# Kernel optimization log

Hardware: AMD Instinct MI355X
Metric: run time of the kernel (lower is better)

Reference implementation:

```python
import jax, jax.numpy as jnp
from jax import lax
import numpy as np

B, T, C, V, E, H, OC = 1024, 32, 14, 21128, 200, 50, 8


def gru(x, Wih, Whh, bih, bhh):
    # x: [N, T, E] -> hiddens [N, T, H]; torch nn.GRU gate order (r, z, n)
    Hd = Whh.shape[1]
    xp = jnp.einsum('nte,ge->ntg', x, Wih) + bih  # [N, T, 3H]
    h0 = jnp.zeros((x.shape[0], Hd), x.dtype)

    def step(h, xt):
        gh = h @ Whh.T + bhh
        r = jax.nn.sigmoid(xt[:, :Hd] + gh[:, :Hd])
        z = jax.nn.sigmoid(xt[:, Hd:2 * Hd] + gh[:, Hd:2 * Hd])
        n = jnp.tanh(xt[:, 2 * Hd:] + r * gh[:, 2 * Hd:])
        h_new = (1.0 - z) * n + z * h
        return h_new, h_new

    _, hs = lax.scan(step, h0, jnp.swapaxes(xp, 0, 1))
    return jnp.swapaxes(hs, 0, 1)


def setup_inputs():
    key = jax.random.key(0)
    ks = jax.random.split(key, 32)
    s = 0.1
    inp = {
        'contexts_indices': jax.random.randint(ks[0], (B, T), 0, V),
        'candidates_indices': jax.random.randint(ks[1], (B, C, T), 0, V),
        'y_dev': jax.random.uniform(ks[2], (B, C), dtype=jnp.float32),
        'emb': jax.random.normal(ks[3], (V, E), dtype=jnp.float32),
        'A': jax.random.normal(ks[4], (H, H), dtype=jnp.float32) * s,
        'Wih_c': jax.random.normal(ks[5], (3 * H, E), dtype=jnp.float32) * s,
        'Whh_c': jax.random.normal(ks[6], (3 * H, H), dtype=jnp.float32) * s,
        'bih_c': jnp.zeros((3 * H,), jnp.float32),
        'bhh_c': jnp.zeros((3 * H,), jnp.float32),
        'Wih_r': jax.random.normal(ks[7], (3 * H, E), dtype=jnp.float32) * s,
        'Whh_r': jax.random.normal(ks[8], (3 * H, H), dtype=jnp.float32) * s,
        'bih_r': jnp.zeros((3 * H,), jnp.float32),
        'bhh_r': jnp.zeros((3 * H,), jnp.float32),
        'conv_w': jax.random.normal(ks[9], (OC, 2, 3, 3), dtype=jnp.float32) * s,
        'Wih2': jax.random.normal(ks[10], (3 * H, OC * 10 * 10), dtype=jnp.float32) * s,
        'Whh2': jax.random.normal(ks[11], (3 * H, H), dtype=jnp.float32) * s,
        'bih2': jnp.zeros((3 * H,), jnp.float32),
        'bhh2': jnp.zeros((3 * H,), jnp.float32),
        'fc1_w': jax.random.normal(ks[12], (100, C * H), dtype=jnp.float32) * s,
        'fc1_b': jnp.zeros((100,), jnp.float32),
        'fc2_w': jax.random.normal(ks[13], (C, 100), dtype=jnp.float32) * s,
        'fc2_b': jnp.zeros((C,), jnp.float32),
    }
    return inp


def reference(contexts_indices, candidates_indices, y_dev, emb, A,
              Wih_c, Whh_c, bih_c, bhh_c, Wih_r, Whh_r, bih_r, bhh_r,
              conv_w, Wih2, Whh2, bih2, bhh2, fc1_w, fc1_b, fc2_w, fc2_b):
    b = contexts_indices.shape[0]
    ctx = contexts_indices[:, None, :]                      # [B,1,T]
    ctx_emb = emb[ctx]                                      # [B,1,T,E] (dropout = identity in eval)
    cand_emb = emb[candidates_indices]                      # [B,C,T,E]

    ctx_h = gru(ctx_emb.reshape(-1, T, E), Wih_c, Whh_c, bih_c, bhh_c).reshape(b, 1, T, H)
    cand_h = gru(cand_emb.reshape(-1, T, E), Wih_r, Whh_r, bih_r, bhh_r).reshape(b, C, T, H)

    M1 = jnp.einsum('btph,bcqh->btcpq', ctx_emb, cand_emb)  # [B,1,C,T,T]
    ctx_hA = jnp.einsum('btij,jk->btik', ctx_h, A)
    M2 = jnp.einsum('btph,bcqh->btcpq', ctx_hA, cand_h)

    # faithful to torch: stack on dim 2 then row-major view(-1, 2, T, T)
    M = jnp.stack([M1, M2], axis=2).reshape(-1, 2, T, T)    # [B*C, 2, T, T]

    conv = lax.conv_general_dilated(M, conv_w, (1, 1), 'VALID',
                                    dimension_numbers=('NCHW', 'OIHW', 'NCHW'))  # [B*C, OC, 30, 30]
    pooled = lax.reduce_window(conv, -jnp.inf, lax.max,
                               (1, 1, 3, 3), (1, 1, 3, 3), 'VALID')              # [B*C, OC, 10, 10]

    feats = pooled.reshape(b, C, OC * 10 * 10)              # [B, C, 800]
    Hs = gru(feats, Wih2, Whh2, bih2, bhh2)                 # [B, C, H]
    flat = Hs.reshape(b, -1)                                # [B, C*H]

    hid = jax.nn.relu(flat @ fc1_w.T + fc1_b)
    log_probs = jax.nn.log_softmax(hid @ fc2_w.T + fc2_b, axis=-1)  # softmax then log
    kl = jnp.where(y_dev > 0, y_dev * (jnp.log(y_dev) - log_probs), 0.0)
    return jnp.mean(kl)
```

## Files before the change

kernel.cpp:

```cpp
#include <hip/hip_runtime.h>
#include <math.h>

typedef unsigned short u16;
typedef short s16;
typedef u16 u16x8 __attribute__((ext_vector_type(8)));
typedef s16 short8v __attribute__((ext_vector_type(8)));
typedef float f32x4 __attribute__((ext_vector_type(4)));

__device__ __forceinline__ float b2f(u16 u) {
    return __uint_as_float(((unsigned)u) << 16);
}
__device__ __forceinline__ u16 f2b(float f) {
    unsigned u = __float_as_uint(f);
    unsigned r = (u + 0x7FFFu + ((u >> 16) & 1u)) >> 16;
    return (u16)r;
}

__global__ __launch_bounds__(256) void k_cvt_all(
    const float* __restrict__ emb, u16* __restrict__ embh,
    const float* __restrict__ wcf, u16* __restrict__ wch,
    const float* __restrict__ wrf, u16* __restrict__ wrh,
    const float* __restrict__ w2f, u16* __restrict__ w2h)
{
    long j = (long)blockIdx.x * 256 + threadIdx.x;
    if (j < 1056400) {
        float4 v = ((const float4*)emb)[j];
        *(ushort4*)(embh + j * 4) = make_ushort4(f2b(v.x), f2b(v.y), f2b(v.z), f2b(v.w));
        return;
    }
    j -= 1056400;
    if (j < 7500) {
        float4 v = ((const float4*)wcf)[j];
        *(ushort4*)(wch + j * 4) = make_ushort4(f2b(v.x), f2b(v.y), f2b(v.z), f2b(v.w));
        return;
    }
    j -= 7500;
    if (j < 7500) {
        float4 v = ((const float4*)wrf)[j];
        *(ushort4*)(wrh + j * 4) = make_ushort4(f2b(v.x), f2b(v.y), f2b(v.z), f2b(v.w));
        return;
    }
    j -= 7500;
    if (j < 120000) {
        int jj = (int)(j / 800), k = (int)(j % 800);
        int p = k >> 3, oc = k & 7;
        w2h[jj * 800 + k] = f2b(w2f[jj * 800 + oc * 100 + p]);
    }
}

__global__ __launch_bounds__(256) void k_projmm2(
    const u16* __restrict__ embh, const u16* __restrict__ wc,
    const u16* __restrict__ wr, const float* __restrict__ bc,
    const float* __restrict__ br, u16* __restrict__ outc,
    u16* __restrict__ outr, int V)
{
    __shared__ s16 Ab[2048];
    __shared__ s16 Bb[2560];
    __shared__ float bhL[160];
    const int t = threadIdx.x;
    const int w = t >> 6, l = t & 63, lg = l >> 4, lr = l & 15;
    int id = blockIdx.x;
    const int half = (id >= 662) ? 1 : 0;
    id -= half * 662;
    const u16* wh = half ? wr : wc;
    const float* bias = half ? br : bc;
    u16* outp = half ? outr : outc;
    const int mb = id >> 1, nb = id & 1;
    const long rowbase = (long)mb * 64;
    const int colbase = nb * 80;
    if (t < 160) bhL[t] = (t < 150) ? bias[t] : 0.f;

    f32x4 acc[5];
#pragma unroll
    for (int i = 0; i < 5; ++i) acc[i] = (f32x4){0,0,0,0};

    for (int ch = 0; ch < 7; ++ch) {
        __syncthreads();
        {
            int kc = t >> 6, row = t & 63;
            long grow = rowbase + row; if (grow >= V) grow = V - 1;
            int k0 = ch * 32 + kc * 8;
            short8v v = {0,0,0,0,0,0,0,0};
            if (k0 < 200) v = *(const short8v*)(embh + grow * 200 + k0);
            *(short8v*)&Ab[t * 8] = v;
        }
        for (int it = t; it < 320; it += 256) {
            int kc = it / 80, col = it % 80;
            int gcol = colbase + col;
            int k0 = ch * 32 + kc * 8;
            short8v v = {0,0,0,0,0,0,0,0};
            if (gcol < 150 && k0 < 200)
                v = *(const short8v*)(wh + (size_t)gcol * 200 + k0);
            *(short8v*)&Bb[it * 8] = v;
        }
        __syncthreads();
        short8v a = *(short8v*)&Ab[(lg * 64 + w * 16 + lr) * 8];
#pragma unroll
        for (int ct = 0; ct < 5; ++ct) {
            short8v bv = *(short8v*)&Bb[(lg * 80 + ct * 16 + lr) * 8];
            acc[ct] = __builtin_amdgcn_mfma_f32_16x16x32_bf16(a, bv, acc[ct], 0, 0, 0);
        }
    }
#pragma unroll
    for (int ct = 0; ct < 5; ++ct) {
        int gcol = colbase + ct * 16 + lr;
        if (gcol < 150) {
#pragma unroll
            for (int rr = 0; rr < 4; ++rr) {
                long row = rowbase + w * 16 + lg * 4 + rr;
                outp[row * 152 + gcol] = f2b(acc[ct][rr] + bhL[gcol]);
            }
        }
    }
}

template<int MODE, int SEQS>
__device__ __forceinline__ void gru_body(
    char* sm, const void* __restrict__ xp_, const int* __restrict__ idx,
    const float* __restrict__ Whh, const float* __restrict__ bhh,
    void* __restrict__ hs_, int T, long blk)
{
    s16*   hbuf = (s16*)sm;
    float* ghL  = (float*)(sm + 2048);
    float* hL   = (float*)(sm + 2048 + SEQS * 640);
    float* bhL  = (float*)(sm + 2048 + SEQS * 848);
    u16*   xraw = (u16*)(sm + 2048 + SEQS * 848 + 608);
    const int t = threadIdx.x;
    const int w = t >> 6, l = t & 63, lg = l >> 4, lr = l & 15;
    constexpr int HST = (MODE == 2) ? 56 : 50;
    constexpr int XROW = SEQS * 152;
    u16*   xbH = xraw;
    float* xbF = (float*)xraw;

    for (int li = t; li < 1024; li += 256) hbuf[li] = 0;
    for (int e = t; e < SEQS * 52; e += 256) hL[e] = 0.f;
    if (t < 152) bhL[t] = (t < 150) ? bhh[t] : 0.f;

    const int te_0 = (w * 3     > 9) ? 9 : w * 3;
    const int te_1 = (w * 3 + 1 > 9) ? 9 : w * 3 + 1;
    const int te_2 = (w * 3 + 2 > 9) ? 9 : w * 3 + 2;
    short8v B00 = {0,0,0,0,0,0,0,0}, B01 = B00, B10 = B00, B11 = B00, B20 = B00, B21 = B00;
    {
        int cols[3] = { te_0 * 16 + lr, te_1 * 16 + lr, te_2 * 16 + lr };
        short8v* frg[6] = { &B00, &B01, &B10, &B11, &B20, &B21 };
#pragma unroll
        for (int ti = 0; ti < 3; ++ti) {
            int col = cols[ti];
            if (col < 150) {
#pragma unroll
                for (int s = 0; s < 2; ++s) {
                    short8v v = {0,0,0,0,0,0,0,0};
#pragma unroll
                    for (int e = 0; e < 8; ++e) {
                        int k = (s * 4 + lg) * 8 + e;
                        if (k < 50) v[e] = (s16)f2b(Whh[col * 50 + k]);
                    }
                    *frg[ti * 2 + s] = v;
                }
            }
        }
    }

    const long seqbase = blk * SEQS;
    const float* xpf = (const float*)xp_;
    const u16*   xph = (const u16*)xp_;
    float* hsf = (float*)hs_;
    u16*   hsh = (u16*)hs_;

    const int rA = (MODE == 2) ? t / 19 : t / 38;
    const int oA = (MODE == 2) ? (t % 19) * 8 : (t % 38) * 4;
    const int rB = (MODE == 2) ? (t + 256) / 19 : (t + 256) / 38;
    const int oB = (MODE == 2) ? ((t + 256) % 19) * 8 : ((t + 256) % 38) * 4;
    const bool actA = (MODE == 2) ? (t < SEQS * 19) : true;
    const bool hasB = (MODE == 2) ? (t + 256 < SEQS * 19) : (t + 256 < SEQS * 38);

    auto rowbase = [&](int rr, int stp) -> size_t {
        long r = seqbase + rr;
        long src = (MODE == 0) ? (r * T + stp) : (long)idx[r * T + stp];
        return (size_t)src * 152;
    };

    if (MODE == 2) {
        if (actA) *(u16x8*)&xbH[rA * 152 + oA] = *(const u16x8*)(xph + rowbase(rA, 0) + oA);
        if (hasB) *(u16x8*)&xbH[rB * 152 + oB] = *(const u16x8*)(xph + rowbase(rB, 0) + oB);
    } else {
        *(float4*)&xbF[rA * 152 + oA] = *(const float4*)(xpf + rowbase(rA, 0) + oA);
        if (hasB)
            *(float4*)&xbF[rB * 152 + oB] = *(const float4*)(xpf + rowbase(rB, 0) + oB);
    }
    __syncthreads();

    for (int st = 0; st < T; ++st) {
        const int cur = st & 1;
        u16x8 pfh0, pfh1;
        float4 pf0, pf1;
        if (st + 1 < T) {
            if (MODE == 2) {
                if (actA) pfh0 = *(const u16x8*)(xph + rowbase(rA, st + 1) + oA);
                if (hasB) pfh1 = *(const u16x8*)(xph + rowbase(rB, st + 1) + oB);
            } else {
                pf0 = *(const float4*)(xpf + rowbase(rA, st + 1) + oA);
                if (hasB) pf1 = *(const float4*)(xpf + rowbase(rB, st + 1) + oB);
            }
        }
        short8v a0 = *(short8v*)&hbuf[((0 + lg) * 16 + lr) * 8];
        short8v a1 = *(short8v*)&hbuf[((4 + lg) * 16 + lr) * 8];
        f32x4 c0 = {0,0,0,0}, c1 = {0,0,0,0}, c2 = {0,0,0,0};
        c0 = __builtin_amdgcn_mfma_f32_16x16x32_bf16(a0, B00, c0, 0, 0, 0);
        c0 = __builtin_amdgcn_mfma_f32_16x16x32_bf16(a1, B01, c0, 0, 0, 0);
        c1 = __builtin_amdgcn_mfma_f32_16x16x32_bf16(a0, B10, c1, 0, 0, 0);
        c1 = __builtin_amdgcn_mfma_f32_16x16x32_bf16(a1, B11, c1, 0, 0, 0);
        c2 = __builtin_amdgcn_mfma_f32_16x16x32_bf16(a0, B20, c2, 0, 0, 0);
        c2 = __builtin_amdgcn_mfma_f32_16x16x32_bf16(a1, B21, c2, 0, 0, 0);
        if (lg * 4 < SEQS) {
            int col0 = te_0 * 16 + lr, col1 = te_1 * 16 + lr, col2 = te_2 * 16 + lr;
            if (col0 < 150) {
#pragma unroll
                for (int r = 0; r < 4; ++r) ghL[(lg * 4 + r) * 160 + col0] = c0[r] + bhL[col0];
            }
            if (col1 < 150) {
#pragma unroll
                for (int r = 0; r < 4; ++r) ghL[(lg * 4 + r) * 160 + col1] = c1[r] + bhL[col1];
            }
            if (col2 < 150) {
#pragma unroll
                for (int r = 0; r < 4; ++r) ghL[(lg * 4 + r) * 160 + col2] = c2[r] + bhL[col2];
            }
        }
        __syncthreads();
        if (st + 1 < T) {
            if (MODE == 2) {
                if (actA) *(u16x8*)&xbH[(cur ^ 1) * XROW + rA * 152 + oA] = pfh0;
                if (hasB) *(u16x8*)&xbH[(cur ^ 1) * XROW + rB * 152 + oB] = pfh1;
            } else {
                *(float4*)&xbF[(cur ^ 1) * XROW + rA * 152 + oA] = pf0;
                if (hasB) *(float4*)&xbF[(cur ^ 1) * XROW + rB * 152 + oB] = pf1;
            }
        }
        for (int item = t; item < SEQS * 50; item += 256) {
            int ss = item / 50, hh = item % 50;
            float xv0, xv1, xv2;
            if (MODE == 2) {
                const u16* xr = &xbH[cur * XROW + ss * 152];
                xv0 = b2f(xr[hh]); xv1 = b2f(xr[50 + hh]); xv2 = b2f(xr[100 + hh]);
            } else {
                const float* xr = &xbF[cur * XROW + ss * 152];
                xv0 = xr[hh]; xv1 = xr[50 + hh]; xv2 = xr[100 + hh];
            }
            float vr  = xv0 + ghL[ss * 160 + hh];
            float vz  = xv1 + ghL[ss * 160 + 50 + hh];
            float ghn = ghL[ss * 160 + 100 + hh];
            float rg = 1.f / (1.f + __expf(-vr));
            float zg = 1.f / (1.f + __expf(-vz));
            float a = xv2 + rg * ghn;
            a = fminf(fmaxf(a, -15.f), 15.f);
            float e2 = __expf(-2.f * a);
            float nn2 = (1.f - e2) / (1.f + e2);
            float hn = (1.f - zg) * nn2 + zg * hL[ss * 52 + hh];
            hL[ss * 52 + hh] = hn;
            hbuf[((hh >> 3) * 16 + ss) * 8 + (hh & 7)] = (s16)f2b(hn);
            size_t ofs = ((size_t)(seqbase + ss) * T + st) * HST + hh;
            if (MODE == 2) hsh[ofs] = f2b(hn); else hsf[ofs] = hn;
        }
        __syncthreads();
    }
}

__device__ __forceinline__ void conv_pool_epi(
    char* sm, u16* __restrict__ feats, long nl, f32x4 cacc0, f32x4 cacc1)
{
    s16* pool16 = (s16*)sm;
    float* wL = (float*)(sm + 18960);
    u16* Mb    = (u16*)pool16;
    u16* convL = (u16*)pool16 + 2184;
    const int t = threadIdx.x;
    const int w = t >> 6, l = t & 63, lg = l >> 4, lr = l & 15;
    const int job0 = w * 2, job1 = w * 2 + 1;
    const int ch0 = job0 >> 2, rt0 = (job0 >> 1) & 1, ct0 = job0 & 1;
    const int ch1 = job1 >> 2, rt1 = (job1 >> 1) & 1, ct1 = job1 & 1;

    __syncthreads();
#pragma unroll
    for (int rr = 0; rr < 4; ++rr) {
        Mb[ch0 * 1092 + (rt0 * 16 + lg * 4 + rr) * 33 + ct0 * 16 + lr] = f2b(cacc0[rr]);
        Mb[ch1 * 1092 + (rt1 * 16 + lg * 4 + rr) * 33 + ct1 * 16 + lr] = f2b(cacc1[rr]);
    }

    short8v Bc = {0,0,0,0,0,0,0,0};
    int dlt[8];
#pragma unroll
    for (int e = 0; e < 8; ++e) {
        int s = lg * 8 + e;
        if (s < 18) {
            int ch = s / 9, r9 = s % 9, ky = r9 / 3, kx = r9 % 3;
            dlt[e] = ch * 1092 + ky * 33 + kx;
            if (lr < 8) Bc[e] = (s16)f2b(wL[lr * 18 + s]);
        } else dlt[e] = 0;
    }
    __syncthreads();

    for (int tile = w; tile < 57; tile += 4) {
        int m = tile * 16 + lr;
        int cy = m / 30, cx = m - cy * 30;
        int base = cy * 33 + cx;
        short8v a;
#pragma unroll
        for (int e = 0; e < 8; ++e) a[e] = (s16)Mb[base + dlt[e]];
        f32x4 c = {0,0,0,0};
        c = __builtin_amdgcn_mfma_f32_16x16x32_bf16(a, Bc, c, 0, 0, 0);
        if (lr < 8) {
#pragma unroll
            for (int rr = 0; rr < 4; ++rr)
                convL[(tile * 16 + lg * 4 + rr) * 8 + lr] = f2b(c[rr]);
        }
    }
    __syncthreads();

    if (t < 100) {
        int py = t / 10, px = t % 10;
        int m0 = (3 * py) * 30 + 3 * px;
        float mx[8];
#pragma unroll
        for (int c = 0; c < 8; ++c) mx[c] = -1e30f;
#pragma unroll
        for (int dy = 0; dy < 3; ++dy)
#pragma unroll
            for (int dx = 0; dx < 3; ++dx) {
                u16x8 v = *(u16x8*)&convL[(m0 + dy * 30 + dx) * 8];
#pragma unroll
                for (int c = 0; c < 8; ++c) mx[c] = fmaxf(mx[c], b2f(v[c]));
            }
        u16x8 o;
#pragma unroll
        for (int c = 0; c < 8; ++c) o[c] = f2b(mx[c]);
        *(u16x8*)(feats + nl * 800 + t * 8) = o;
    }
}

__device__ __forceinline__ void conv_pool_epi2(
    s16* pool, short8v Bc, const int* dlt,
    u16* __restrict__ feats, long nl, f32x4 cacc0, f32x4 cacc1)
{
    u16* Mb    = (u16*)pool;
    u16* convL = (u16*)pool + 2184;
    const int t = threadIdx.x;
    const int w = t >> 6, l = t & 63, lg = l >> 4, lr = l & 15;
    const int job0 = w * 2, job1 = w * 2 + 1;
    const int ch0 = job0 >> 2, rt0 = (job0 >> 1) & 1, ct0 = job0 & 1;
    const int ch1 = job1 >> 2, rt1 = (job1 >> 1) & 1, ct1 = job1 & 1;

    __syncthreads();
#pragma unroll
    for (int rr = 0; rr < 4; ++rr) {
        Mb[ch0 * 1092 + (rt0 * 16 + lg * 4 + rr) * 33 + ct0 * 16 + lr] = f2b(cacc0[rr]);
        Mb[ch1 * 1092 + (rt1 * 16 + lg * 4 + rr) * 33 + ct1 * 16 + lr] = f2b(cacc1[rr]);
    }
    __syncthreads();

    for (int tile = w; tile < 29; tile += 4) {
        int m = tile * 16 + lr;
        int cy = m / 30, cx = m - cy * 30;
        int base = cy * 33 + cx;
        short8v a;
#pragma unroll
        for (int e = 0; e < 8; ++e) a[e] = (s16)Mb[base + dlt[e]];
        f32x4 c = {0,0,0,0};
        c = __builtin_amdgcn_mfma_f32_16x16x32_bf16(a, Bc, c, 0, 0, 0);
        if (lr < 8) {
#pragma unroll
            for (int rr = 0; rr < 4; ++rr)
                convL[(tile * 16 + lg * 4 + rr) * 8 + lr] = f2b(c[rr]);
        }
    }
    __syncthreads();
    if (t < 50) {
        int py = t / 10, px = t % 10;
        int m0 = (3 * py) * 30 + 3 * px;
        float mx[8];
#pragma unroll
        for (int c = 0; c < 8; ++c) mx[c] = -1e30f;
#pragma unroll
        for (int dy = 0; dy < 3; ++dy)
#pragma unroll
            for (int dx = 0; dx < 3; ++dx) {
                u16x8 v = *(u16x8*)&convL[(m0 + dy * 30 + dx) * 8];
#pragma unroll
                for (int c = 0; c < 8; ++c) mx[c] = fmaxf(mx[c], b2f(v[c]));
            }
        u16x8 o;
#pragma unroll
        for (int c = 0; c < 8; ++c) o[c] = f2b(mx[c]);
        *(u16x8*)(feats + nl * 800 + t * 8) = o;
    }
    __syncthreads();
    for (int tile = 28 + w; tile < 57; tile += 4) {
        int m = tile * 16 + lr;
        int cy = m / 30, cx = m - cy * 30;
        int base = cy * 33 + cx;
        short8v a;
#pragma unroll
        for (int e = 0; e < 8; ++e) a[e] = (s16)Mb[base + dlt[e]];
        f32x4 c = {0,0,0,0};
        c = __builtin_amdgcn_mfma_f32_16x16x32_bf16(a, Bc, c, 0, 0, 0);
        if (lr < 8) {
#pragma unroll
            for (int rr = 0; rr < 4; ++rr)
                convL[(tile * 16 + lg * 4 + rr - 448) * 8 + lr] = f2b(c[rr]);
        }
    }
    __syncthreads();
    if (t < 50) {
        int py = 5 + t / 10, px = t % 10;
        int m0 = (3 * py) * 30 + 3 * px - 448;
        float mx[8];
#pragma unroll
        for (int c = 0; c < 8; ++c) mx[c] = -1e30f;
#pragma unroll
        for (int dy = 0; dy < 3; ++dy)
#pragma unroll
            for (int dx = 0; dx < 3; ++dx) {
                u16x8 v = *(u16x8*)&convL[(m0 + dy * 30 + dx) * 8];
#pragma unroll
                for (int c = 0; c < 8; ++c) mx[c] = fmaxf(mx[c], b2f(v[c]));
            }
        u16x8 o;
#pragma unroll
        for (int c = 0; c < 8; ++c) o[c] = f2b(mx[c]);
        *(u16x8*)(feats + nl * 800 + (50 + t) * 8) = o;
    }
    __syncthreads();
}

__device__ __forceinline__ void m1_body(
    char* sm, const u16* __restrict__ embh, const int* __restrict__ ctx_idx,
    const int* __restrict__ cand_idx, const float* __restrict__ conv_w,
    u16* __restrict__ feats, int wg)
{
    s16* pool16 = (s16*)sm;
    float* wL = (float*)(sm + 18960);
    int* ci = (int*)(sm + 19536);
    int* qi = (int*)(sm + 19664);
    const int t = threadIdx.x;
    const int xcd = wg & 7, q = wg >> 3;
    const int r = q % 7, bq = q / 7;
    const int b = bq * 8 + xcd;
    const long nl = (long)b * 14 + r;
    const int w = t >> 6, l = t & 63, lg = l >> 4, lr = l & 15;

    if (t < 144) wL[t] = conv_w[t];

    f32x4 cacc0 = {0,0,0,0}, cacc1 = {0,0,0,0};
    const int job0 = w * 2, job1 = w * 2 + 1;
    const int ch0 = job0 >> 2, rt0 = (job0 >> 1) & 1, ct0 = job0 & 1;
    const int ch1 = job1 >> 2, rt1 = (job1 >> 1) & 1, ct1 = job1 & 1;

    const int c0 = 2 * r;
    if (t < 32) ci[t] = ctx_idx[b * 32 + t];
    else if (t < 96)
        qi[((t - 32) >> 5) * 32 + (t & 31)] =
            cand_idx[((long)b * 14 + c0 + ((t - 32) >> 5)) * 32 + (t & 31)];
    __syncthreads();
    s16* ctxL = pool16;
    s16* canL = pool16 + 3168;
#pragma unroll
    for (int cnk = 0; cnk < 3; ++cnk) {
        const int kcbase = (cnk == 0) ? 0 : (cnk == 1 ? 12 : 20);
        const int kccnt  = (cnk == 0) ? 12 : 8;
        const int scnt   = (cnk == 0) ? 3 : 2;
        if (cnk) __syncthreads();
        for (int it = t; it < kccnt * 32; it += 256) {
            int kcl = it >> 5, row = it & 31;
            int kc = kcbase + kcl;
            short8v v = {0,0,0,0,0,0,0,0};
            if (kc < 25) v = *(const short8v*)(embh + (size_t)ci[row] * 200 + kc * 8);
            *(short8v*)&ctxL[(kcl * 33 + row) * 8] = v;
        }
        for (int it = t; it < kccnt * 64; it += 256) {
            int kcl = it >> 6, col = it & 63;
            int kc = kcbase + kcl;
            short8v v = {0,0,0,0,0,0,0,0};
            if (kc < 25)
                v = *(const short8v*)(embh + (size_t)qi[(col >> 5) * 32 + (col & 31)] * 200 + kc * 8);
            *(short8v*)&canL[(kcl * 65 + col) * 8] = v;
        }
        __syncthreads();
        for (int sl = 0; sl < scnt; ++sl) {
            int kcl = sl * 4 + lg;
            short8v a0 = *(short8v*)&ctxL[(kcl * 33 + rt0 * 16 + lr) * 8];
            short8v b0 = *(short8v*)&canL[(kcl * 65 + ch0 * 32 + ct0 * 16 + lr) * 8];
            short8v b1 = *(short8v*)&canL[(kcl * 65 + ch1 * 32 + ct1 * 16 + lr) * 8];
            cacc0 = __builtin_amdgcn_mfma_f32_16x16x32_bf16(a0, b0, cacc0, 0, 0, 0);
            short8v a1 = (rt0 == rt1) ? a0
                       : *(short8v*)&ctxL[(kcl * 33 + rt1 * 16 + lr) * 8];
            cacc1 = __builtin_amdgcn_mfma_f32_16x16x32_bf16(a1, b1, cacc1, 0, 0, 0);
        }
    }
    conv_pool_epi(sm, feats, nl, cacc0, cacc1);
}

__global__ __launch_bounds__(256) void k_scan_m1(
    const u16* __restrict__ proj_ch, const u16* __restrict__ proj_rh,
    const int* __restrict__ ctx_idx, const int* __restrict__ cand_idx,
    const float* __restrict__ Whh_c, const float* __restrict__ Whh_r,
    const float* __restrict__ bhh_c, const float* __restrict__ bhh_r,
    u16* __restrict__ ctx_hh, u16* __restrict__ candh_h,
    const u16* __restrict__ embh, const float* __restrict__ conv_w,
    u16* __restrict__ feats)
{
    __shared__ long long smq[3244];
    char* sm = (char*)smq;
    const long bid = blockIdx.x;
    if (bid < 960) {
        const bool cand = (bid < 896);
        gru_body<2, 16>(sm,
                        cand ? (const void*)proj_rh : (const void*)proj_ch,
                        cand ? cand_idx : ctx_idx,
                        cand ? Whh_r : Whh_c,
                        cand ? bhh_r : bhh_c,
                        cand ? (void*)candh_h : (void*)ctx_hh,
                        32, cand ? bid : bid - 896);
    } else {
        m1_body(sm, embh, ctx_idx, cand_idx, conv_w, feats, (int)(bid - 960));
    }
}

__global__ __launch_bounds__(256) void k_m2conv(
    const u16* __restrict__ ctxA_h, const u16* __restrict__ candh_h,
    const float* __restrict__ conv_w, u16* __restrict__ feats)
{
    __shared__ long long smq[1640];
    char* sm = (char*)smq;
    s16* aL = (s16*)sm;
    s16* cL = (s16*)sm + 2112;
    float* wL = (float*)(sm + 12544);
    const int t = threadIdx.x;
    const int wg = blockIdx.x;
    const int xcd = wg & 7, q = wg >> 3;
    const int r7 = q % 7, bq = q / 7;
    const int b = bq * 8 + xcd;
    const long nl = (long)b * 14 + 7 + r7;
    const int w = t >> 6, l = t & 63, lg = l >> 4, lr = l & 15;

    if (t < 144) wL[t] = conv_w[t];

    f32x4 cacc0 = {0,0,0,0}, cacc1 = {0,0,0,0};
    const int job0 = w * 2, job1 = w * 2 + 1;
    const int ch0 = job0 >> 2, rt0 = (job0 >> 1) & 1, ct0 = job0 & 1;
    const int ch1 = job1 >> 2, rt1 = (job1 >> 1) & 1, ct1 = job1 & 1;

    const int c0 = 2 * r7;
    for (int it = t; it < 256; it += 256) {
        int kc = it >> 5, row = it & 31;
        short8v v = {0,0,0,0,0,0,0,0};
        if (kc < 7) {
            v = *(const short8v*)(ctxA_h + (size_t)(b * 32 + row) * 56 + kc * 8);
            if (kc == 6) { v[2] = 0; v[3] = 0; v[4] = 0; v[5] = 0; v[6] = 0; v[7] = 0; }
        }
        *(short8v*)&aL[(kc * 33 + row) * 8] = v;
    }
    for (int it = t; it < 512; it += 256) {
        int kc = it >> 6, col = it & 63;
        long row = ((long)b * 14 + c0 + (col >> 5)) * 32 + (col & 31);
        short8v v = {0,0,0,0,0,0,0,0};
        if (kc < 7) {
            v = *(const short8v*)(candh_h + (size_t)row * 56 + kc * 8);
            if (kc == 6) { v[2] = 0; v[3] = 0; v[4] = 0; v[5] = 0; v[6] = 0; v[7] = 0; }
        }
        *(short8v*)&cL[(kc * 65 + col) * 8] = v;
    }
    __syncthreads();

    short8v Bc = {0,0,0,0,0,0,0,0};
    int dlt[8];
#pragma unroll
    for (int e = 0; e < 8; ++e) {
        int s = lg * 8 + e;
        if (s < 18) {
            int ch = s / 9, r9 = s % 9, ky = r9 / 3, kx = r9 % 3;
            dlt[e] = ch * 1092 + ky * 33 + kx;
            if (lr < 8) Bc[e] = (s16)f2b(wL[lr * 18 + s]);
        } else dlt[e] = 0;
    }

#pragma unroll
    for (int sl = 0; sl < 2; ++sl) {
        int kcl = sl * 4 + lg;
        short8v a0 = *(short8v*)&aL[(kcl * 33 + rt0 * 16 + lr) * 8];
        short8v b0 = *(short8v*)&cL[(kcl * 65 + ch0 * 32 + ct0 * 16 + lr) * 8];
        short8v b1 = *(short8v*)&cL[(kcl * 65 + ch1 * 32 + ct1 * 16 + lr) * 8];
        cacc0 = __builtin_amdgcn_mfma_f32_16x16x32_bf16(a0, b0, cacc0, 0, 0, 0);
        short8v a1 = (rt0 == rt1) ? a0
                   : *(short8v*)&aL[(kcl * 33 + rt1 * 16 + lr) * 8];
        cacc1 = __builtin_amdgcn_mfma_f32_16x16x32_bf16(a1, b1, cacc1, 0, 0, 0);
    }
    conv_pool_epi2((s16*)sm, Bc, dlt, feats, nl, cacc0, cacc1);
}

__global__ __launch_bounds__(256) void k_scan2(
    const float* __restrict__ xp2, const float* __restrict__ Whh2,
    const float* __restrict__ bhh2, float* __restrict__ hs2)
{
    __shared__ long long smq[2396];
    gru_body<0, 8>((char*)smq, xp2, nullptr, Whh2, bhh2, hs2, 14, (long)blockIdx.x);
}

__global__ __launch_bounds__(256) void k_matA(
    const u16* __restrict__ inh, const float* __restrict__ A,
    u16* __restrict__ outh)
{
    __shared__ float AL[50 * 52];
    __shared__ float inL[32 * 52];
    const int t = threadIdx.x;
    for (int e = t; e < 2500; e += 256) AL[(e / 50) * 52 + (e % 50)] = A[e];
    const long rbase = (long)blockIdx.x * 32;
    for (int e = t; e < 1600; e += 256) {
        int r = e / 50, j = e % 50;
        inL[r * 52 + j] = b2f(inh[(rbase + r) * 56 + j]);
    }
    __syncthreads();
    for (int item = t; item < 1600; item += 256) {
        int r = item / 50, kk = item % 50;
        float acc = 0.f;
#pragma unroll 10
        for (int j = 0; j < 50; ++j)
            acc += inL[r * 52 + j] * AL[j * 52 + kk];
        outh[(rbase + r) * 56 + kk] = f2b(acc);
    }
}

__global__ __launch_bounds__(256) void k_xp2mm(
    const u16* __restrict__ feats, const u16* __restrict__ w2h,
    const float* __restrict__ bih2, float* __restrict__ out)
{
    __shared__ s16 Ab[2048];
    __shared__ s16 Bb[2560];
    __shared__ float bhL[160];
    const int t = threadIdx.x;
    const int w = t >> 6, l = t & 63, lg = l >> 4, lr = l & 15;
    const int mb = blockIdx.x >> 1, nb = blockIdx.x & 1;
    const long rowbase = (long)mb * 64;
    const int colbase = nb * 80;
    if (t < 160) bhL[t] = (t < 150) ? bih2[t] : 0.f;

    f32x4 acc[5];
#pragma unroll
    for (int i = 0; i < 5; ++i) acc[i] = (f32x4){0,0,0,0};

    for (int ch = 0; ch < 25; ++ch) {
        __syncthreads();
        {
            int kc = t >> 6, row = t & 63;
            *(short8v*)&Ab[t * 8] =
                *(const short8v*)(feats + (rowbase + row) * 800 + ch * 32 + kc * 8);
        }
        for (int it = t; it < 320; it += 256) {
            int kc = it / 80, col = it % 80;
            int gcol = colbase + col;
            short8v v = {0,0,0,0,0,0,0,0};
            if (gcol < 150)
                v = *(const short8v*)(w2h + (size_t)gcol * 800 + ch * 32 + kc * 8);
            *(short8v*)&Bb[it * 8] = v;
        }
        __syncthreads();
        short8v a = *(short8v*)&Ab[(lg * 64 + w * 16 + lr) * 8];
#pragma unroll
        for (int ct = 0; ct < 5; ++ct) {
            short8v bv = *(short8v*)&Bb[(lg * 80 + ct * 16 + lr) * 8];
            acc[ct] = __builtin_amdgcn_mfma_f32_16x16x32_bf16(a, bv, acc[ct], 0, 0, 0);
        }
    }
#pragma unroll
    for (int ct = 0; ct < 5; ++ct) {
        int gcol = colbase + ct * 16 + lr;
        if (gcol < 150) {
#pragma unroll
            for (int rr = 0; rr < 4; ++rr) {
                long row = rowbase + w * 16 + lg * 4 + rr;
                out[row * 152 + gcol] = acc[ct][rr] + bhL[gcol];
            }
        }
    }
}

__global__ __launch_bounds__(128) void k_head(
    const float* __restrict__ Hs, const float* __restrict__ w1,
    const float* __restrict__ b1, const float* __restrict__ w2,
    const float* __restrict__ b2, const float* __restrict__ y,
    float* __restrict__ partial)
{
    __shared__ float hr[700];
    __shared__ float hidL[100];
    const int t = threadIdx.x;
    const long b = blockIdx.x;
    for (int e = t; e < 700; e += 128) hr[e] = Hs[b * 700 + e];
    __syncthreads();
    if (t < 100) {
        float acc = b1[t];
        const float4* wp = (const float4*)(w1 + (size_t)t * 700);
        for (int k4 = 0; k4 < 175; ++k4) {
            float4 wv = wp[k4];
            float4 hv = *(float4*)&hr[k4 * 4];
            acc += wv.x * hv.x + wv.y * hv.y + wv.z * hv.z + wv.w * hv.w;
        }
        hidL[t] = fmaxf(acc, 0.f);
    }
    __syncthreads();
    if (t < 64) {
        float logit = -1e30f;
        if (t < 14) {
            logit = b2[t];
            for (int k = 0; k < 100; ++k) logit += hidL[k] * w2[t * 100 + k];
        }
        float m = logit;
        for (int off = 8; off; off >>= 1) m = fmaxf(m, __shfl_xor(m, off, 16));
        float ex = (t < 14) ? __expf(logit - m) : 0.f;
        float se = ex;
        for (int off = 8; off; off >>= 1) se += __shfl_xor(se, off, 16);
        float kl = 0.f;
        if (t < 14) {
            float lp = logit - m - __logf(se);
            float yv = y[b * 14 + t];
            kl = (yv > 0.f) ? yv * (__logf(yv) - lp) : 0.f;
        }
        for (int off = 8; off; off >>= 1) kl += __shfl_xor(kl, off, 16);
        if (t == 0) partial[b] = kl;
    }
}

__global__ __launch_bounds__(256) void k_reduce(
    const float* __restrict__ partial, float* __restrict__ out)
{
    __shared__ float sm[256];
    const int t = threadIdx.x;
    sm[t] = partial[t] + partial[t + 256] + partial[t + 512] + partial[t + 768];
    __syncthreads();
    for (int off = 128; off; off >>= 1) {
        if (t < off) sm[t] += sm[t + off];
        __syncthreads();
    }
    if (t == 0) out[0] = sm[0] * (1.f / 14336.f);
}

extern "C" void kernel_launch(void* const* d_in, const int* in_sizes, int n_in,
                              void* d_out, int out_size, void* d_ws, size_t ws_size,
                              hipStream_t stream)
{
    const int*   ctx_idx  = (const int*)d_in[0];
    const int*   cand_idx = (const int*)d_in[1];
    const float* y_dev    = (const float*)d_in[2];
    const float* emb      = (const float*)d_in[3];
    const float* A        = (const float*)d_in[4];
    const float* Wih_c    = (const float*)d_in[5];
    const float* Whh_c    = (const float*)d_in[6];
    const float* bih_c    = (const float*)d_in[7];
    const float* bhh_c    = (const float*)d_in[8];
    const float* Wih_r    = (const float*)d_in[9];
    const float* Whh_r    = (const float*)d_in[10];
    const float* bih_r    = (const float*)d_in[11];
    const float* bhh_r    = (const float*)d_in[12];
    const float* conv_w   = (const float*)d_in[13];
    const float* Wih2     = (const float*)d_in[14];
    const float* Whh2     = (const float*)d_in[15];
    const float* bih2     = (const float*)d_in[16];
    const float* bhh2     = (const float*)d_in[17];
    const float* fc1_w    = (const float*)d_in[18];
    const float* fc1_b    = (const float*)d_in[19];
    const float* fc2_w    = (const float*)d_in[20];
    const float* fc2_b    = (const float*)d_in[21];

    float* ws = (float*)d_ws;
    u16*   embh    = (u16*)ws;
    u16*   proj_ch = (u16*)(ws + 2112800);
    u16*   proj_rh = (u16*)(ws + 3722784);
    u16*   ctx_hh  = (u16*)(ws + 5332768);
    u16*   ctxA_h  = (u16*)(ws + 6250272);
    u16*   candh_h = (u16*)(ws + 7167776);
    u16*   feats_h = (u16*)(ws + 20012832);
    u16*   w2h     = (u16*)(ws + 25747232);
    u16*   wch     = (u16*)(ws + 25807232);
    u16*   wrh     = (u16*)(ws + 25822232);
    float* xp2     = ws + 25837232;
    float* hs2     = ws + 28016304;
    float* part    = ws + 28733104;

    k_cvt_all <<<4654, 256, 0, stream>>>(emb, embh, Wih_c, wch, Wih_r, wrh,
                                         Wih2, w2h);
    k_projmm2 <<<1324, 256, 0, stream>>>(embh, wch, wrh, bih_c, bih_r,
                                         proj_ch, proj_rh, 21128);
    k_scan_m1 <<<8128, 256, 0, stream>>>(proj_ch, proj_rh, ctx_idx, cand_idx,
                                         Whh_c, Whh_r, bhh_c, bhh_r,
                                         ctx_hh, candh_h, embh, conv_w, feats_h);
    k_matA <<<1024, 256, 0, stream>>>(ctx_hh, A, ctxA_h);
    k_m2conv <<<7168, 256, 0, stream>>>(ctxA_h, candh_h, conv_w, feats_h);
    k_xp2mm <<<448, 256, 0, stream>>>(feats_h, w2h, bih2, xp2);
    k_scan2 <<<128, 256, 0, stream>>>(xp2, Whh2, bhh2, hs2);
    k_head <<<1024, 128, 0, stream>>>(hs2, fc1_w, fc1_b, fc2_w, fc2_b, y_dev, part);
    k_reduce <<<1, 256, 0, stream>>>(part, (float*)d_out);
}
```

Measured before the change: 305.2 us.

## Fuse matA into ctx GRU blocks and split xp2 GEMM across m2conv launch

Moves the ctx_h @ A multiply into the tail of the 64 context-GRU blocks of k_scan_m1, which removes the separate k_matA launch. The xp2 input projection is split by candidate index: rows for candidates 0-6 (whose M1/M2 features are already complete) run as extra blocks inside the m2conv launch, and the remaining rows run in a smaller follow-up kernel. Global-to-LDS load indexing is also reordered so consecutive threads read contiguous 16-byte chunks of the same row, for better coalescing. The trade-off is that only 64 blocks do the serialized matA tail, which may lengthen the scan kernel's critical path.

```diff
diff --git a/kernel.cpp b/kernel.cpp
--- a/kernel.cpp
+++ b/kernel.cpp
@@ -77,21 +77,21 @@
     for (int ch = 0; ch < 7; ++ch) {
         __syncthreads();
         {
-            int kc = t >> 6, row = t & 63;
+            int row = t >> 2, kc = t & 3;
             long grow = rowbase + row; if (grow >= V) grow = V - 1;
             int k0 = ch * 32 + kc * 8;
             short8v v = {0,0,0,0,0,0,0,0};
             if (k0 < 200) v = *(const short8v*)(embh + grow * 200 + k0);
-            *(short8v*)&Ab[t * 8] = v;
+            *(short8v*)&Ab[(kc * 64 + row) * 8] = v;
         }
         for (int it = t; it < 320; it += 256) {
-            int kc = it / 80, col = it % 80;
+            int col = it >> 2, kc = it & 3;
             int gcol = colbase + col;
             int k0 = ch * 32 + kc * 8;
             short8v v = {0,0,0,0,0,0,0,0};
             if (gcol < 150 && k0 < 200)
                 v = *(const short8v*)(wh + (size_t)gcol * 200 + k0);
-            *(short8v*)&Bb[it * 8] = v;
+            *(short8v*)&Bb[(kc * 80 + col) * 8] = v;
         }
         __syncthreads();
         short8v a = *(short8v*)&Ab[(lg * 64 + w * 16 + lr) * 8];
@@ -266,6 +266,34 @@
     }
 }
 
+__device__ __forceinline__ void matA_tail(
+    char* sm, const u16* __restrict__ ctx_hh, const float* __restrict__ A,
+    u16* __restrict__ ctxA_h, long blk)
+{
+    float* AL  = (float*)sm;
+    float* inL = (float*)(sm + 10400);
+    const int t = threadIdx.x;
+    for (int e = t; e < 2500; e += 256) AL[(e / 50) * 52 + (e % 50)] = A[e];
+    const long rbase0 = blk * 512;
+    for (int c16 = 0; c16 < 16; ++c16) {
+        __syncthreads();
+        const long rbase = rbase0 + c16 * 32;
+        for (int e = t; e < 1600; e += 256) {
+            int r = e / 50, j = e % 50;
+            inL[r * 52 + j] = b2f(ctx_hh[(rbase + r) * 56 + j]);
+        }
+        __syncthreads();
+        for (int item = t; item < 1600; item += 256) {
+            int r = item / 50, kk = item % 50;
+            float acc = 0.f;
+#pragma unroll 10
+            for (int j = 0; j < 50; ++j)
+                acc += inL[r * 52 + j] * AL[j * 52 + kk];
+            ctxA_h[(rbase + r) * 56 + kk] = f2b(acc);
+        }
+    }
+}
+
 __device__ __forceinline__ void conv_pool_epi(
     char* sm, u16* __restrict__ feats, long nl, f32x4 cacc0, f32x4 cacc1)
 {
@@ -469,14 +497,14 @@
         const int scnt   = (cnk == 0) ? 3 : 2;
         if (cnk) __syncthreads();
         for (int it = t; it < kccnt * 32; it += 256) {
-            int kcl = it >> 5, row = it & 31;
+            int row = it / kccnt, kcl = it - row * kccnt;
             int kc = kcbase + kcl;
             short8v v = {0,0,0,0,0,0,0,0};
             if (kc < 25) v = *(const short8v*)(embh + (size_t)ci[row] * 200 + kc * 8);
             *(short8v*)&ctxL[(kcl * 33 + row) * 8] = v;
         }
         for (int it = t; it < kccnt * 64; it += 256) {
-            int kcl = it >> 6, col = it & 63;
+            int col = it / kccnt, kcl = it - col * kccnt;
             int kc = kcbase + kcl;
             short8v v = {0,0,0,0,0,0,0,0};
             if (kc < 25)
@@ -505,7 +533,8 @@
     const float* __restrict__ bhh_c, const float* __restrict__ bhh_r,
     u16* __restrict__ ctx_hh, u16* __restrict__ candh_h,
     const u16* __restrict__ embh, const float* __restrict__ conv_w,
-    u16* __restrict__ feats)
+    u16* __restrict__ feats, const float* __restrict__ A,
+    u16* __restrict__ ctxA_h)
 {
     __shared__ long long smq[3244];
     char* sm = (char*)smq;
@@ -519,23 +548,85 @@
                         cand ? bhh_r : bhh_c,
                         cand ? (void*)candh_h : (void*)ctx_hh,
                         32, cand ? bid : bid - 896);
+        if (!cand) matA_tail(sm, ctx_hh, A, ctxA_h, bid - 896);
     } else {
         m1_body(sm, embh, ctx_idx, cand_idx, conv_w, feats, (int)(bid - 960));
     }
 }
 
-__global__ __launch_bounds__(256) void k_m2conv(
+__device__ __forceinline__ void xp2_body(
+    char* sm, const u16* __restrict__ feats, const u16* __restrict__ w2h,
+    const float* __restrict__ bih2, float* __restrict__ out, int id2, int rlo)
+{
+    s16* Ab = (s16*)sm;
+    s16* Bb = (s16*)sm + 4608;
+    float* bhL = (float*)(sm + 14336);
+    const int t = threadIdx.x;
+    const int w = t >> 6, l = t & 63, lg = l >> 4, lr = l & 15;
+    const int btile = id2 / 14, rem = id2 % 14;
+    const int rr = rlo + rem / 2, nb = rem % 2;
+    const int colbase = nb * 80;
+    if (t < 160) bhL[t] = (t < 150) ? bih2[t] : 0.f;
+
+    f32x4 acc[5];
+#pragma unroll
+    for (int i = 0; i < 5; ++i) acc[i] = (f32x4){0,0,0,0};
+
+    for (int ch = 0; ch < 25; ++ch) {
+        __syncthreads();
+        {
+            int row = t >> 2, kc = t & 3;
+            long n = ((long)btile * 64 + row) * 14 + rr;
+            *(short8v*)&Ab[(kc * 64 + row) * 8] =
+                *(const short8v*)(feats + n * 800 + ch * 32 + kc * 8);
+        }
+        for (int it = t; it < 320; it += 256) {
+            int col = it >> 2, kc = it & 3;
+            int gcol = colbase + col;
+            short8v v = {0,0,0,0,0,0,0,0};
+            if (gcol < 150)
+                v = *(const short8v*)(w2h + (size_t)gcol * 800 + ch * 32 + kc * 8);
+            *(short8v*)&Bb[(kc * 80 + col) * 8] = v;
+        }
+        __syncthreads();
+        short8v a = *(short8v*)&Ab[(lg * 64 + w * 16 + lr) * 8];
+#pragma unroll
+        for (int ct = 0; ct < 5; ++ct) {
+            short8v bv = *(short8v*)&Bb[(lg * 80 + ct * 16 + lr) * 8];
+            acc[ct] = __builtin_amdgcn_mfma_f32_16x16x32_bf16(a, bv, acc[ct], 0, 0, 0);
+        }
+    }
+#pragma unroll
+    for (int ct = 0; ct < 5; ++ct) {
+        int gcol = colbase + ct * 16 + lr;
+        if (gcol < 150) {
+#pragma unroll
+            for (int rr4 = 0; rr4 < 4; ++rr4) {
+                long n = ((long)btile * 64 + w * 16 + lg * 4 + rr4) * 14 + rr;
+                out[n * 152 + gcol] = acc[ct][rr4] + bhL[gcol];
+            }
+        }
+    }
+}
+
+__global__ __launch_bounds__(256) void k_m2x(
     const u16* __restrict__ ctxA_h, const u16* __restrict__ candh_h,
-    const float* __restrict__ conv_w, u16* __restrict__ feats)
-{
-    __shared__ long long smq[1640];
+    const float* __restrict__ conv_w, u16* __restrict__ feats,
+    const u16* __restrict__ w2h, const float* __restrict__ bih2,
+    float* __restrict__ xp2)
+{
+    __shared__ long long smq[1872];
     char* sm = (char*)smq;
+    const int bid = blockIdx.x;
+    if (bid >= 7168) {
+        xp2_body(sm, feats, w2h, bih2, xp2, bid - 7168, 0);
+        return;
+    }
     s16* aL = (s16*)sm;
     s16* cL = (s16*)sm + 2112;
     float* wL = (float*)(sm + 12544);
     const int t = threadIdx.x;
-    const int wg = blockIdx.x;
-    const int xcd = wg & 7, q = wg >> 3;
+    const int xcd = bid & 7, q = bid >> 3;
     const int r7 = q % 7, bq = q / 7;
     const int b = bq * 8 + xcd;
     const long nl = (long)b * 14 + 7 + r7;
@@ -550,7 +641,7 @@
 
     const int c0 = 2 * r7;
     for (int it = t; it < 256; it += 256) {
-        int kc = it >> 5, row = it & 31;
+        int row = it >> 3, kc = it & 7;
         short8v v = {0,0,0,0,0,0,0,0};
         if (kc < 7) {
             v = *(const short8v*)(ctxA_h + (size_t)(b * 32 + row) * 56 + kc * 8);
@@ -559,7 +650,7 @@
         *(short8v*)&aL[(kc * 33 + row) * 8] = v;
     }
     for (int it = t; it < 512; it += 256) {
-        int kc = it >> 6, col = it & 63;
+        int col = it >> 3, kc = it & 7;
         long row = ((long)b * 14 + c0 + (col >> 5)) * 32 + (col & 31);
         short8v v = {0,0,0,0,0,0,0,0};
         if (kc < 7) {
@@ -596,90 +687,20 @@
     conv_pool_epi2((s16*)sm, Bc, dlt, feats, nl, cacc0, cacc1);
 }
 
+__global__ __launch_bounds__(256) void k_xp2t(
+    const u16* __restrict__ feats, const u16* __restrict__ w2h,
+    const float* __restrict__ bih2, float* __restrict__ xp2)
+{
+    __shared__ long long smq[1872];
+    xp2_body((char*)smq, feats, w2h, bih2, xp2, (int)blockIdx.x, 7);
+}
+
 __global__ __launch_bounds__(256) void k_scan2(
     const float* __restrict__ xp2, const float* __restrict__ Whh2,
     const float* __restrict__ bhh2, float* __restrict__ hs2)
 {
     __shared__ long long smq[2396];
     gru_body<0, 8>((char*)smq, xp2, nullptr, Whh2, bhh2, hs2, 14, (long)blockIdx.x);
-}
-
-__global__ __launch_bounds__(256) void k_matA(
-    const u16* __restrict__ inh, const float* __restrict__ A,
-    u16* __restrict__ outh)
-{
-    __shared__ float AL[50 * 52];
-    __shared__ float inL[32 * 52];
-    const int t = threadIdx.x;
-    for (int e = t; e < 2500; e += 256) AL[(e / 50) * 52 + (e % 50)] = A[e];
-    const long rbase = (long)blockIdx.x * 32;
-    for (int e = t; e < 1600; e += 256) {
-        int r = e / 50, j = e % 50;
-        inL[r * 52 + j] = b2f(inh[(rbase + r) * 56 + j]);
-    }
-    __syncthreads();
-    for (int item = t; item < 1600; item += 256) {
-        int r = item / 50, kk = item % 50;
-        float acc = 0.f;
-#pragma unroll 10
-        for (int j = 0; j < 50; ++j)
-            acc += inL[r * 52 + j] * AL[j * 52 + kk];
-        outh[(rbase + r) * 56 + kk] = f2b(acc);
-    }
-}
-
-__global__ __launch_bounds__(256) void k_xp2mm(
-    const u16* __restrict__ feats, const u16* __restrict__ w2h,
-    const float* __restrict__ bih2, float* __restrict__ out)
-{
-    __shared__ s16 Ab[2048];
-    __shared__ s16 Bb[2560];
-    __shared__ float bhL[160];
-    const int t = threadIdx.x;
-    const int w = t >> 6, l = t & 63, lg = l >> 4, lr = l & 15;
-    const int mb = blockIdx.x >> 1, nb = blockIdx.x & 1;
-    const long rowbase = (long)mb * 64;
-    const int colbase = nb * 80;
-    if (t < 160) bhL[t] = (t < 150) ? bih2[t] : 0.f;
-
-    f32x4 acc[5];
-#pragma unroll
-    for (int i = 0; i < 5; ++i) acc[i] = (f32x4){0,0,0,0};
-
-    for (int ch = 0; ch < 25; ++ch) {
-        __syncthreads();
-        {
-            int kc = t >> 6, row = t & 63;
-            *(short8v*)&Ab[t * 8] =
-                *(const short8v*)(feats + (rowbase + row) * 800 + ch * 32 + kc * 8);
-        }
-        for (int it = t; it < 320; it += 256) {
-            int kc = it / 80, col = it % 80;
-            int gcol = colbase + col;
-            short8v v = {0,0,0,0,0,0,0,0};
-            if (gcol < 150)
-                v = *(const short8v*)(w2h + (size_t)gcol * 800 + ch * 32 + kc * 8);
-            *(short8v*)&Bb[it * 8] = v;
-        }
-        __syncthreads();
-        short8v a = *(short8v*)&Ab[(lg * 64 + w * 16 + lr) * 8];
-#pragma unroll
-        for (int ct = 0; ct < 5; ++ct) {
-            short8v bv = *(short8v*)&Bb[(lg * 80 + ct * 16 + lr) * 8];
-            acc[ct] = __builtin_amdgcn_mfma_f32_16x16x32_bf16(a, bv, acc[ct], 0, 0, 0);
-        }
-    }
-#pragma unroll
-    for (int ct = 0; ct < 5; ++ct) {
-        int gcol = colbase + ct * 16 + lr;
-        if (gcol < 150) {
-#pragma unroll
-            for (int rr = 0; rr < 4; ++rr) {
-                long row = rowbase + w * 16 + lg * 4 + rr;
-                out[row * 152 + gcol] = acc[ct][rr] + bhL[gcol];
-            }
-        }
-    }
 }
 
 __global__ __launch_bounds__(128) void k_head(
@@ -789,10 +810,11 @@
                                          proj_ch, proj_rh, 21128);
     k_scan_m1 <<<8128, 256, 0, stream>>>(proj_ch, proj_rh, ctx_idx, cand_idx,
                                          Whh_c, Whh_r, bhh_c, bhh_r,
-                                         ctx_hh, candh_h, embh, conv_w, feats_h);
-    k_matA <<<1024, 256, 0, stream>>>(ctx_hh, A, ctxA_h);
-    k_m2conv <<<7168, 256, 0, stream>>>(ctxA_h, candh_h, conv_w, feats_h);
-    k_xp2mm <<<448, 256, 0, stream>>>(feats_h, w2h, bih2, xp2);
+                                         ctx_hh, candh_h, embh, conv_w, feats_h,
+                                         A, ctxA_h);
+    k_m2x <<<7392, 256, 0, stream>>>(ctxA_h, candh_h, conv_w, feats_h,
+                                     w2h, bih2, xp2);
+    k_xp2t <<<224, 256, 0, stream>>>(feats_h, w2h, bih2, xp2);
     k_scan2 <<<128, 256, 0, stream>>>(xp2, Whh2, bhh2, hs2);
     k_head <<<1024, 128, 0, stream>>>(hs2, fc1_w, fc1_b, fc2_w, fc2_b, y_dev, part);
     k_reduce <<<1, 256, 0, stream>>>(part, (float*)d_out);
```

After: 357.2 us. 17.0% more time.
